# Optimization experiments

Measured on AMD Instinct MI355X. Metric: run time of the kernel, lower is better.

The kernel has to match this reference:

```python
import jax, jax.numpy as jnp
import numpy as np

B, D, K = 65536, 256, 10
LOG_2PI = float(np.log(2.0 * np.pi))


def setup_inputs() -> dict:
    key = jax.random.key(0)
    k1, k2 = jax.random.split(key)
    q_z = jax.random.normal(k1, (B, D), dtype=jnp.float32)
    # Xavier-uniform init for mu lookup (approximated with normal scale)
    mu_table = jax.random.normal(k2, (K, D), dtype=jnp.float32) * 0.1
    # logvar lookup initialized to log(exp(0)**2) = 0
    logvar_table = jnp.zeros((K, D), dtype=jnp.float32)
    return {"q_z": q_z, "mu_table": mu_table, "logvar_table": logvar_table}


def reference(q_z, mu_table, logvar_table):
    # q_z: [B, D]; mu_table, logvar_table: [K, D]
    k = mu_table.shape[0]
    diff = q_z[:, None, :] - mu_table[None, :, :]              # [B, K, D]
    llh = -0.5 * (diff * diff / jnp.exp(logvar_table)[None]
                  + logvar_table[None] + LOG_2PI)              # [B, K, D]
    log_q_y_logit = jnp.sum(llh, axis=2) + jnp.log(1.0 / k)    # [B, K]
    q_y = jax.nn.softmax(log_q_y_logit, axis=1)                # [B, K]
    ind = jnp.argmax(q_y, axis=1)                              # [B]
    return (log_q_y_logit, q_y, ind)
```

## Files before the change

### kernel.cpp

```cpp
#include <hip/hip_runtime.h>
#include <hip/hip_bf16.h>
#include <math.h>

#define BB 65536
#define DD 256
#define KK 10
#define LOG_2PI 1.8378770664093453f

__global__ __launch_bounds__(DD) void gmvae_prep(
    const float* __restrict__ mu_table,
    const float* __restrict__ logvar_table,
    float* __restrict__ tab,
    float* __restrict__ C)
{
    const int k = blockIdx.x;
    const int d = threadIdx.x;
    const float lv = logvar_table[k * DD + d];
    const float m  = mu_table[k * DD + d];
    const float iv = expf(-lv);
    const float a  = m * iv;

    const int f    = d >> 2;
    const int s    = f >> 4;
    const int c    = (f >> 2) & 3;
    const int jj   = f & 3;
    const int comp = d & 3;
    const int idx_f4 = ((s * 4 + jj) * KK + k) * 2;
    const int base   = c * 1280 + idx_f4 * 4 + comp;
    tab[base]     = iv;
    tab[base + 4] = -2.0f * a;

    float p = fmaf(m, a, lv);
    __shared__ float red[4];
    #pragma unroll
    for (int off = 32; off > 0; off >>= 1)
        p += __shfl_down(p, off, 64);
    if ((threadIdx.x & 63) == 0)
        red[threadIdx.x >> 6] = p;
    __syncthreads();
    if (threadIdx.x == 0) {
        const float s2 = (red[0] + red[1]) + (red[2] + red[3]);
        C[k] = -0.5f * (s2 + 256.0f * LOG_2PI) + logf(0.1f);
    }
}

__device__ __forceinline__ float rl(float v, int lane) {
    return __int_as_float(__builtin_amdgcn_readlane(__float_as_int(v), lane));
}

__global__ __launch_bounds__(256) void gmvae_main(
    const float* __restrict__ q_z,
    const float* __restrict__ tab,
    const float* __restrict__ C,
    float* __restrict__ out)
{
    __shared__ float4 buf[2 * 64 * 17];
    float* comb = reinterpret_cast<float*>(buf);

    const int t    = threadIdx.x;
    const int r    = t & 63;
    const int c    = __builtin_amdgcn_readfirstlane(t >> 6);
    const int row0 = blockIdx.x * 64;

    const float4* __restrict__ q4 = reinterpret_cast<const float4*>(q_z);

    const float4* __restrict__ t4 =
        reinterpret_cast<const float4*>(tab) + c * 320;
    float4 w[5];
    #pragma unroll
    for (int i = 0; i < 5; ++i)
        w[i] = t4[i * 64 + r];

    const int rr0 = t >> 4;
    const int ff  = t & 15;

    float acc[KK];
    #pragma unroll
    for (int k = 0; k < KK; ++k) acc[k] = 0.f;

    float4 v[4];
    #pragma unroll
    for (int i = 0; i < 4; ++i)
        v[i] = q4[(size_t)(row0 + i * 16 + rr0) * 64 + 0 * 16 + ff];
    #pragma unroll
    for (int i = 0; i < 4; ++i)
        buf[(i * 16 + rr0) * 17 + ff] = v[i];
    __syncthreads();

    #pragma unroll
    for (int s = 0; s < 4; ++s) {
        if (s < 3) {
            #pragma unroll
            for (int i = 0; i < 4; ++i)
                v[i] = q4[(size_t)(row0 + i * 16 + rr0) * 64 + (s + 1) * 16 + ff];
        }

        const float4* bp = buf + (s & 1) * (64 * 17) + r * 17 + c * 4;
        #pragma unroll
        for (int jj = 0; jj < 4; ++jj) {
            const float4 q = bp[jj];
            const float qx2 = q.x * q.x, qy2 = q.y * q.y;
            const float qz2 = q.z * q.z, qw2 = q.w * q.w;
            #pragma unroll
            for (int k = 0; k < KK; ++k) {
                const int flat = ((s * 4 + jj) * KK + k) * 2;
                const int i = flat >> 6;
                const int L = flat & 63;
                const float4 wv = w[i];
                acc[k] = fmaf(qx2, rl(wv.x, L),     acc[k]);
                acc[k] = fmaf(q.x, rl(wv.x, L + 1), acc[k]);
                acc[k] = fmaf(qy2, rl(wv.y, L),     acc[k]);
                acc[k] = fmaf(q.y, rl(wv.y, L + 1), acc[k]);
                acc[k] = fmaf(qz2, rl(wv.z, L),     acc[k]);
                acc[k] = fmaf(q.z, rl(wv.z, L + 1), acc[k]);
                acc[k] = fmaf(qw2, rl(wv.w, L),     acc[k]);
                acc[k] = fmaf(q.w, rl(wv.w, L + 1), acc[k]);
            }
        }

        if (s < 3) {
            float4* wp = buf + ((s + 1) & 1) * (64 * 17);
            #pragma unroll
            for (int i = 0; i < 4; ++i)
                wp[(i * 16 + rr0) * 17 + ff] = v[i];
            __syncthreads();
        }
    }

    __syncthreads();
    #pragma unroll
    for (int k = 0; k < KK; ++k)
        comb[t * 11 + k] = acc[k];
    __syncthreads();

    if (t < 64) {
        float l[KK];
        #pragma unroll
        for (int k = 0; k < KK; ++k) {
            const float vsum =
                ((comb[r * 11 + k]         + comb[(64 + r) * 11 + k]) +
                 (comb[(128 + r) * 11 + k] + comb[(192 + r) * 11 + k]));
            l[k] = fmaf(vsum, -0.5f, C[k]);
        }

        float mx = l[0];
        #pragma unroll
        for (int k = 1; k < KK; ++k) mx = fmaxf(mx, l[k]);

        float e[KK];
        float sum = 0.f;
        #pragma unroll
        for (int k = 0; k < KK; ++k) { e[k] = __expf(l[k] - mx); sum += e[k]; }
        const float inv = 1.0f / sum;

        int idx = 0;
        float best = l[0];
        #pragma unroll
        for (int k = 1; k < KK; ++k)
            if (l[k] > best) { best = l[k]; idx = k; }

        const int row = row0 + r;
        float2* __restrict__ o1 =
            reinterpret_cast<float2*>(out) + (size_t)row * 5;
        float2* __restrict__ o2 =
            reinterpret_cast<float2*>(out + (size_t)BB * KK) + (size_t)row * 5;
        #pragma unroll
        for (int k = 0; k < 5; ++k)
            o1[k] = make_float2(l[2 * k], l[2 * k + 1]);
        #pragma unroll
        for (int k = 0; k < 5; ++k)
            o2[k] = make_float2(e[2 * k] * inv, e[2 * k + 1] * inv);
        out[(size_t)2 * BB * KK + row] = (float)idx;
    }
}

extern "C" void kernel_launch(void* const* d_in, const int* in_sizes, int n_in,
                              void* d_out, int out_size, void* d_ws, size_t ws_size,
                              hipStream_t stream) {
    const float* q_z    = (const float*)d_in[0];
    const float* mu     = (const float*)d_in[1];
    const float* logvar = (const float*)d_in[2];
    float* out = (float*)d_out;

    float* tab = (float*)d_ws;
    float* C   = tab + 5120;

    gmvae_prep<<<KK, DD, 0, stream>>>(mu, logvar, tab, C);
    gmvae_main<<<BB / 64, 256, 0, stream>>>(q_z, tab, C, out);
}
```

Baseline: 104.0 us.

## Split feature dimension across 8 waves and load q_z directly into registers

The main kernel now uses 512 threads per 64-row block, with each of 8 waves covering 32 features per row instead of 4 waves covering 64. Each lane reads its own row's float4s straight from global memory into registers, replacing the LDS double-buffered transpose and the per-stage barriers. The prep kernel's table layout is reordered to match the new 8-chunk split, and the final reduction now sums 8 partials per class. Per-lane loads are strided by row, which gives less coalesced global access in exchange for dropping the LDS traffic and syncs.

```diff
diff --git a/kernel.cpp b/kernel.cpp
--- a/kernel.cpp
+++ b/kernel.cpp
@@ -21,12 +21,10 @@
     const float a  = m * iv;
 
     const int f    = d >> 2;
-    const int s    = f >> 4;
-    const int c    = (f >> 2) & 3;
-    const int jj   = f & 3;
+    const int c    = f >> 3;
+    const int j    = f & 7;
     const int comp = d & 3;
-    const int idx_f4 = ((s * 4 + jj) * KK + k) * 2;
-    const int base   = c * 1280 + idx_f4 * 4 + comp;
+    const int base = c * 640 + ((j * KK + k) * 2) * 4 + comp;
     tab[base]     = iv;
     tab[base + 4] = -2.0f * a;
 
@@ -48,31 +46,28 @@
     return __int_as_float(__builtin_amdgcn_readlane(__float_as_int(v), lane));
 }
 
-__global__ __launch_bounds__(256) void gmvae_main(
+__global__ __launch_bounds__(512) void gmvae_main(
     const float* __restrict__ q_z,
     const float* __restrict__ tab,
     const float* __restrict__ C,
     float* __restrict__ out)
 {
-    __shared__ float4 buf[2 * 64 * 17];
-    float* comb = reinterpret_cast<float*>(buf);
+    __shared__ float comb[512 * 11];
 
     const int t    = threadIdx.x;
     const int r    = t & 63;
     const int c    = __builtin_amdgcn_readfirstlane(t >> 6);
     const int row0 = blockIdx.x * 64;
 
-    const float4* __restrict__ q4 = reinterpret_cast<const float4*>(q_z);
+    const float4* __restrict__ t4 =
+        reinterpret_cast<const float4*>(tab) + c * 160;
+    float4 w[3];
+    w[0] = t4[r];
+    w[1] = t4[64 + r];
+    w[2] = t4[128 + (r & 31)];
 
-    const float4* __restrict__ t4 =
-        reinterpret_cast<const float4*>(tab) + c * 320;
-    float4 w[5];
-    #pragma unroll
-    for (int i = 0; i < 5; ++i)
-        w[i] = t4[i * 64 + r];
-
-    const int rr0 = t >> 4;
-    const int ff  = t & 15;
+    const float4* __restrict__ qp =
+        reinterpret_cast<const float4*>(q_z) + (size_t)(row0 + r) * 64 + c * 8;
 
     float acc[KK];
     #pragma unroll
@@ -80,32 +75,26 @@
 
     float4 v[4];
     #pragma unroll
-    for (int i = 0; i < 4; ++i)
-        v[i] = q4[(size_t)(row0 + i * 16 + rr0) * 64 + 0 * 16 + ff];
-    #pragma unroll
-    for (int i = 0; i < 4; ++i)
-        buf[(i * 16 + rr0) * 17 + ff] = v[i];
-    __syncthreads();
+    for (int i = 0; i < 4; ++i) v[i] = qp[i];
 
     #pragma unroll
-    for (int s = 0; s < 4; ++s) {
-        if (s < 3) {
+    for (int half = 0; half < 2; ++half) {
+        float4 u[4];
+        if (half == 0) {
             #pragma unroll
-            for (int i = 0; i < 4; ++i)
-                v[i] = q4[(size_t)(row0 + i * 16 + rr0) * 64 + (s + 1) * 16 + ff];
+            for (int i = 0; i < 4; ++i) u[i] = qp[4 + i];
         }
-
-        const float4* bp = buf + (s & 1) * (64 * 17) + r * 17 + c * 4;
         #pragma unroll
         for (int jj = 0; jj < 4; ++jj) {
-            const float4 q = bp[jj];
+            const int j = half * 4 + jj;
+            const float4 q = v[jj];
             const float qx2 = q.x * q.x, qy2 = q.y * q.y;
             const float qz2 = q.z * q.z, qw2 = q.w * q.w;
             #pragma unroll
             for (int k = 0; k < KK; ++k) {
-                const int flat = ((s * 4 + jj) * KK + k) * 2;
-                const int i = flat >> 6;
-                const int L = flat & 63;
+                const int p = (j * KK + k) * 2;
+                const int i = p >> 6;
+                const int L = p & 63;
                 const float4 wv = w[i];
                 acc[k] = fmaf(qx2, rl(wv.x, L),     acc[k]);
                 acc[k] = fmaf(q.x, rl(wv.x, L + 1), acc[k]);
@@ -117,17 +106,12 @@
                 acc[k] = fmaf(q.w, rl(wv.w, L + 1), acc[k]);
             }
         }
-
-        if (s < 3) {
-            float4* wp = buf + ((s + 1) & 1) * (64 * 17);
+        if (half == 0) {
             #pragma unroll
-            for (int i = 0; i < 4; ++i)
-                wp[(i * 16 + rr0) * 17 + ff] = v[i];
-            __syncthreads();
+            for (int i = 0; i < 4; ++i) v[i] = u[i];
         }
     }
 
-    __syncthreads();
     #pragma unroll
     for (int k = 0; k < KK; ++k)
         comb[t * 11 + k] = acc[k];
@@ -137,10 +121,13 @@
         float l[KK];
         #pragma unroll
         for (int k = 0; k < KK; ++k) {
-            const float vsum =
-                ((comb[r * 11 + k]         + comb[(64 + r) * 11 + k]) +
-                 (comb[(128 + r) * 11 + k] + comb[(192 + r) * 11 + k]));
-            l[k] = fmaf(vsum, -0.5f, C[k]);
+            float s0 = 0.f, s1 = 0.f;
+            #pragma unroll
+            for (int cc = 0; cc < 4; ++cc) {
+                s0 += comb[((2 * cc)     * 64 + r) * 11 + k];
+                s1 += comb[((2 * cc + 1) * 64 + r) * 11 + k];
+            }
+            l[k] = fmaf(s0 + s1, -0.5f, C[k]);
         }
 
         float mx = l[0];
@@ -186,5 +173,5 @@
     float* C   = tab + 5120;
 
     gmvae_prep<<<KK, DD, 0, stream>>>(mu, logvar, tab, C);
-    gmvae_main<<<BB / 64, 256, 0, stream>>>(q_z, tab, C, out);
+    gmvae_main<<<BB / 64, 512, 0, stream>>>(q_z, tab, C, out);
 }
```

Measured after the change: 105.9 us. No clear change (+1.9%).
